# Kernel tuning notes

Measured on AMD Instinct MI355X. Metric: run time of the kernel, lower is better.

Reference implementation:

```python
import jax, jax.numpy as jnp
import numpy as np

B, S, D_MODEL, H, D_HEAD = 4, 2048, 1024, 16, 64
SCALE = D_HEAD ** -0.5


def setup_inputs() -> dict:
    key = jax.random.key(0)
    ks = jax.random.split(key, 6)
    init = lambda k, shp: jax.random.normal(k, shp, jnp.float32) * (shp[0] ** -0.5)
    Xq = jax.random.normal(ks[0], (B, S, D_MODEL), jnp.float32)
    # pre-softmax bool mask: True = masked (fill -inf) -> causal
    mask_bef = jnp.triu(jnp.ones((S, S), dtype=bool), k=1)
    # post-softmax bool mask: True = zero out that attention weight
    mask_aft = jax.random.bernoulli(ks[1], 0.1, (S, S))
    Wq = init(ks[2], (D_MODEL, H * D_HEAD))
    Wk = init(ks[3], (D_MODEL, H * D_HEAD))
    Wv = init(ks[4], (D_MODEL, H * D_HEAD))
    Wo = init(ks[5], (H * D_HEAD, D_MODEL))
    return {"Xq": Xq, "mask_bef": mask_bef, "mask_aft": mask_aft,
            "Wq": Wq, "Wk": Wk, "Wv": Wv, "Wo": Wo}


def reference(Xq, mask_bef, mask_aft, Wq, Wk, Wv, Wo):
    # Self-attention: Xk = Xv = Xq
    def split_heads(X, W):  # [B,S,D] @ [D,H*d] -> [B,H,S,d]
        return (X @ W).reshape(B, S, H, D_HEAD).transpose(0, 2, 1, 3)

    Q = split_heads(Xq, Wq)
    K = split_heads(Xq, Wk)
    V = split_heads(Xq, Wv)
    # scores: [B,H,Sq,Sk]
    scores = jnp.einsum('bhqd,bhkd->bhqk', Q, K) * SCALE
    scores = jnp.where(mask_bef, -jnp.inf, scores)  # pre-softmax bool mask
    attn = jax.nn.softmax(scores, axis=-1)
    attn = jnp.where(mask_aft, 0.0, attn)           # post-softmax bool mask
    out = jnp.einsum('bhqk,bhkd->bhqd', attn, V)    # [B,H,S,d]
    out = out.transpose(0, 2, 1, 3).reshape(B, S, H * D_HEAD)
    return out @ Wo  # [B,S,out_dim_o]
```

## Files before the change

### kernel.cpp

```cpp
#include <hip/hip_runtime.h>
#include <hip/hip_bf16.h>


using bf16 = __hip_bfloat16;
typedef __attribute__((ext_vector_type(8))) short short8;
typedef __attribute__((ext_vector_type(4))) float floatx4;

#define kB 4
#define kS 2048
#define kDM 1024
#define kH 16
#define kDH 64
#define kHeadElems ((size_t)kB * kH * kS * kDH)
#define STR 72

#if __has_builtin(__builtin_amdgcn_exp2f)
#define EXP2(x) __builtin_amdgcn_exp2f(x)
#else
#define EXP2(x) __expf((x) * 0.69314718056f)
#endif

__device__ __forceinline__ unsigned short f2bf(float f) {
    union { float f; unsigned u; } x{f};
    unsigned r = x.u + 0x7fff + ((x.u >> 16) & 1);
    return (unsigned short)(r >> 16);
}
__device__ __forceinline__ void gl_lds16(const void* g, void* l) {
    __builtin_amdgcn_global_load_lds(
        (const __attribute__((address_space(1))) unsigned int*)g,
        (__attribute__((address_space(3))) unsigned int*)l, 16, 0, 0);
}

__global__ __launch_bounds__(256)
void pack_em(const int* __restrict__ mask_aft, unsigned short* __restrict__ EM)
{
    const size_t i = ((size_t)blockIdx.x * 256 + threadIdx.x) * 8;
    const int q  = (int)(i >> 11);
    const int k0 = (int)(i & 2047);
    const int4 m0 = *(const int4*)(mask_aft + i);
    const int4 m1 = *(const int4*)(mask_aft + i + 4);
    union { unsigned short u[8]; uint4 v; } o;
    o.u[0] = (m0.x || (k0 + 0) > q) ? 0 : 0xFFFFu;
    o.u[1] = (m0.y || (k0 + 1) > q) ? 0 : 0xFFFFu;
    o.u[2] = (m0.z || (k0 + 2) > q) ? 0 : 0xFFFFu;
    o.u[3] = (m0.w || (k0 + 3) > q) ? 0 : 0xFFFFu;
    o.u[4] = (m1.x || (k0 + 4) > q) ? 0 : 0xFFFFu;
    o.u[5] = (m1.y || (k0 + 5) > q) ? 0 : 0xFFFFu;
    o.u[6] = (m1.z || (k0 + 6) > q) ? 0 : 0xFFFFu;
    o.u[7] = (m1.w || (k0 + 7) > q) ? 0 : 0xFFFFu;
    *(uint4*)(EM + i) = o.v;
}

__global__ __launch_bounds__(256)
void conv_x(const float* __restrict__ X, bf16* __restrict__ Xb)
{
    const size_t i = ((size_t)blockIdx.x * 256 + threadIdx.x) * 8;
    const float4 a = *(const float4*)(X + i);
    const float4 b = *(const float4*)(X + i + 4);
    union { unsigned short u[8]; uint4 v; } o;
    o.u[0] = f2bf(a.x); o.u[1] = f2bf(a.y); o.u[2] = f2bf(a.z); o.u[3] = f2bf(a.w);
    o.u[4] = f2bf(b.x); o.u[5] = f2bf(b.y); o.u[6] = f2bf(b.z); o.u[7] = f2bf(b.w);
    *(uint4*)(Xb + i) = o.v;
}

__global__ __launch_bounds__(256)
void conv_wT(const float* __restrict__ W, bf16* __restrict__ WT)
{
    __shared__ unsigned short Ls[64][STR];
    const int k0 = blockIdx.x * 64, n0 = blockIdx.y * 64;
    const int tid = threadIdx.x;
    const int r16 = tid >> 4, c4 = (tid & 15) * 4;
    #pragma unroll
    for (int it = 0; it < 4; ++it) {
        const int r = it * 16 + r16;
        const float4 v = *(const float4*)(W + (size_t)(k0 + r) * kDM + n0 + c4);
        Ls[c4 + 0][r] = f2bf(v.x); Ls[c4 + 1][r] = f2bf(v.y);
        Ls[c4 + 2][r] = f2bf(v.z); Ls[c4 + 3][r] = f2bf(v.w);
    }
    __syncthreads();
    #pragma unroll
    for (int it = 0; it < 4; ++it) {
        const int rn = it * 16 + r16;
        ushort4 u;
        u.x = Ls[rn][c4 + 0]; u.y = Ls[rn][c4 + 1];
        u.z = Ls[rn][c4 + 2]; u.w = Ls[rn][c4 + 3];
        *(ushort4*)(WT + (size_t)(n0 + rn) * kDM + k0 + c4) = u;
    }
}

__global__ __launch_bounds__(256)
void qkv_mfma(const bf16* __restrict__ A, const bf16* __restrict__ BT,
              bf16* __restrict__ ws)
{
    __shared__ __align__(16) unsigned short At[128][32];
    __shared__ __align__(16) unsigned short Bt[128][32];
    const int tid = threadIdx.x;
    const int w = tid >> 6, lane = tid & 63;
    const int quad = (tid >> 4) & 3, col = tid & 15;
    const int wm = w >> 1, wn = w & 1;
    const int n0 = blockIdx.x * 128;
    const int m0 = blockIdx.y * 128;

    const bf16* pA = A  + (size_t)(m0 + w * 32 + (lane >> 2)) * kDM + (lane & 3) * 8;
    const bf16* pB = BT + (size_t)(n0 + w * 32 + (lane >> 2)) * kDM + (lane & 3) * 8;
    unsigned short* lA = &At[w * 32][0];
    unsigned short* lB = &Bt[w * 32][0];

    floatx4 acc[4][4];
    #pragma unroll
    for (int i = 0; i < 4; ++i)
        #pragma unroll
        for (int j = 0; j < 4; ++j) acc[i][j] = (floatx4){0.f, 0.f, 0.f, 0.f};

    for (int k0 = 0; k0 < kDM; k0 += 32) {
        __syncthreads();
        gl_lds16(pA + k0, lA);
        gl_lds16(pA + k0 + 16 * kDM, lA + 16 * 32);
        gl_lds16(pB + k0, lB);
        gl_lds16(pB + k0 + 16 * kDM, lB + 16 * 32);
        __syncthreads();
        short8 aA[4], bB[4];
        #pragma unroll
        for (int i = 0; i < 4; ++i)
            aA[i] = *(const short8*)&At[wm * 64 + i * 16 + col][quad * 8];
        #pragma unroll
        for (int j = 0; j < 4; ++j)
            bB[j] = *(const short8*)&Bt[wn * 64 + j * 16 + col][quad * 8];
        #pragma unroll
        for (int i = 0; i < 4; ++i)
            #pragma unroll
            for (int j = 0; j < 4; ++j)
                acc[i][j] = __builtin_amdgcn_mfma_f32_16x16x32_bf16(aA[i], bB[j], acc[i][j], 0, 0, 0);
    }

    const int p  = n0 >> 10;
    const int nn = n0 & 1023;
    const float scl = (p == 0) ? 0.18033688f : 1.0f;
    bf16* Out = ws + (size_t)p * kHeadElems;
    #pragma unroll
    for (int i = 0; i < 4; ++i) {
        #pragma unroll
        for (int r = 0; r < 4; ++r) {
            const int m = m0 + wm * 64 + i * 16 + quad * 4 + r;
            const int b = m >> 11, s = m & 2047;
            #pragma unroll
            for (int j = 0; j < 4; ++j) {
                const int n = nn + wn * 64 + j * 16 + col;
                const int h = n >> 6, d = n & 63;
                Out[((size_t)(b * kH + h) * kS + s) * kDH + d] = __float2bfloat16(acc[i][j][r] * scl);
            }
        }
    }
}

__global__ __launch_bounds__(256)
void vtrans(const bf16* __restrict__ V, bf16* __restrict__ VT)
{
    const int bh = blockIdx.y;
    const int s0 = blockIdx.x * 64;
    const bf16* src = V + (size_t)bh * kS * kDH;
    bf16* dst = VT + (size_t)bh * kS * kDH;
    __shared__ unsigned short L[64][STR];
    const int tid = threadIdx.x;
    #pragma unroll
    for (int t = 0; t < 2; ++t) {
        const int idx = t * 256 + tid;
        const int r = idx >> 3, c8 = (idx & 7) * 8;
        *(uint4*)&L[r][c8] = *(const uint4*)(src + (size_t)(s0 + r) * kDH + c8);
    }
    __syncthreads();
    #pragma unroll
    for (int t = 0; t < 2; ++t) {
        const int idx = t * 256 + tid;
        const int d = idx >> 3, sc = (idx & 7) * 8;
        unsigned short tmp[8];
        #pragma unroll
        for (int e = 0; e < 8; ++e) tmp[e] = L[sc + e][d];
        *(uint4*)(dst + (size_t)d * kS + s0 + sc) = *(uint4*)tmp;
    }
}

__global__ __launch_bounds__(256, 3)
void attn_mfma(const bf16* __restrict__ ws, const bf16* __restrict__ VT,
               const unsigned short* __restrict__ EM,
               bf16* __restrict__ Aout)
{
    const int flat = blockIdx.x + blockIdx.y * 16;
    const int xcd = flat & 7;
    const int idx = flat >> 3;
    const int bh  = xcd * 8 + (idx & 7);
    const int j   = idx >> 3;
    const int qtile = (j & 1) ? (j >> 1) : (15 - (j >> 1));
    const int q0 = qtile * 128;

    const int b = bh >> 4, h = bh & 15;
    const int tid  = threadIdx.x;
    const int w    = tid >> 6;
    const int lane = tid & 63;
    const int quad = (tid >> 4) & 3;
    const int col  = tid & 15;

    const size_t ho = (size_t)bh * kS * kDH;
    const bf16* Qg  = ws + ho;
    const bf16* Kg  = ws + kHeadElems + ho;
    const bf16* VTg = VT + ho;

    __shared__ __align__(16) unsigned short Ks[2][64][64];
    __shared__ __align__(16) unsigned short Vs[2][64][64];
    __shared__ __align__(16) unsigned short Pw[4][2][16][STR];

    const int qw = q0 + w * 32;
    const int swz = col & 7;
    const int sch = (lane & 7) ^ (lane >> 3);

    short8 bQ[2][2];
    const unsigned short* EMq[2];
    #pragma unroll
    for (int sub = 0; sub < 2; ++sub) {
        const bf16* qrow = Qg + (size_t)(qw + sub * 16 + col) * kDH;
        bQ[sub][0] = *(const short8*)(qrow + quad * 8);
        bQ[sub][1] = *(const short8*)(qrow + 32 + quad * 8);
        EMq[sub] = EM + (size_t)(qw + sub * 16 + col) * kS;
    }

    floatx4 Ov[2][4];
    #pragma unroll
    for (int sub = 0; sub < 2; ++sub)
        #pragma unroll
        for (int dg = 0; dg < 4; ++dg) Ov[sub][dg] = (floatx4){0.f, 0.f, 0.f, 0.f};
    float lacc[2] = {0.f, 0.f};

    const int nt = qtile * 2 + 2;

    auto STAGE = [&](int buf, int kt) {
        const bf16* Kt = Kg  + (size_t)(kt * 64) * kDH;
        const bf16* Vt = VTg + kt * 64;
        #pragma unroll
        for (int t = 0; t < 2; ++t) {
            const int rbase = (t * 4 + w) * 8;
            const int r = rbase + (lane >> 3);
            gl_lds16(Kt + (size_t)r * kDH + sch * 8, &Ks[buf][rbase][0]);
            gl_lds16(Vt + (size_t)r * kS  + sch * 8, &Vs[buf][rbase][0]);
        }
    };

    STAGE(0, 0);
    asm volatile("s_waitcnt vmcnt(0)" ::: "memory");
    __builtin_amdgcn_s_barrier();
    __builtin_amdgcn_sched_barrier(0);

    int cur = 0;
    for (int kt = 0; kt < nt; ++kt) {
        if (kt + 1 < nt) STAGE(cur ^ 1, kt + 1);

        const int kt64 = kt * 64;
        if (kt64 <= qw + 31) {
            floatx4 sg[2][4];
            __builtin_amdgcn_s_setprio(1);
            #pragma unroll
            for (int g = 0; g < 4; ++g) {
                const int krow = g * 16 + col;
                const short8 aK0 = *(const short8*)&Ks[cur][krow][(quad ^ swz) * 8];
                const short8 aK1 = *(const short8*)&Ks[cur][krow][((4 + quad) ^ swz) * 8];
                floatx4 sA = {0.f, 0.f, 0.f, 0.f}, sB = {0.f, 0.f, 0.f, 0.f};
                sA = __builtin_amdgcn_mfma_f32_16x16x32_bf16(aK0, bQ[0][0], sA, 0, 0, 0);
                sA = __builtin_amdgcn_mfma_f32_16x16x32_bf16(aK1, bQ[0][1], sA, 0, 0, 0);
                sB = __builtin_amdgcn_mfma_f32_16x16x32_bf16(aK0, bQ[1][0], sB, 0, 0, 0);
                sB = __builtin_amdgcn_mfma_f32_16x16x32_bf16(aK1, bQ[1][1], sB, 0, 0, 0);
                sg[0][g] = sA; sg[1][g] = sB;
            }
            __builtin_amdgcn_s_setprio(0);

            #pragma unroll
            for (int sub = 0; sub < 2; ++sub) {
                const int qbase = qw + sub * 16;
                const bool needC = (kt64 + 63 > qbase);
                float lc = 0.f;
                #pragma unroll
                for (int g = 0; g < 4; ++g) {
                    const float p0 = EXP2(sg[sub][g][0]);
                    const float p1 = EXP2(sg[sub][g][1]);
                    const float p2 = EXP2(sg[sub][g][2]);
                    const float p3 = EXP2(sg[sub][g][3]);
                    if (needC) {
                        const int kb = kt64 + g * 16 + quad * 4;
                        const int qme = qbase + col;
                        lc += (kb + 0 <= qme) ? p0 : 0.f;
                        lc += (kb + 1 <= qme) ? p1 : 0.f;
                        lc += (kb + 2 <= qme) ? p2 : 0.f;
                        lc += (kb + 3 <= qme) ? p3 : 0.f;
                    } else {
                        lc += (p0 + p1) + (p2 + p3);
                    }
                    const unsigned b0 = __float_as_uint(p0) + 0x8000u;
                    const unsigned b1 = __float_as_uint(p1) + 0x8000u;
                    const unsigned b2 = __float_as_uint(p2) + 0x8000u;
                    const unsigned b3 = __float_as_uint(p3) + 0x8000u;
                    uint2 pk;
                    pk.x = __builtin_amdgcn_perm(b1, b0, 0x07060302u);
                    pk.y = __builtin_amdgcn_perm(b3, b2, 0x07060302u);
                    const uint2 em = *(const uint2*)(EMq[sub] + kt64 + g * 16 + quad * 4);
                    pk.x &= em.x; pk.y &= em.y;
                    *(uint2*)&Pw[w][sub][col][g * 16 + quad * 4] = pk;
                }
                lacc[sub] += lc;
            }

            const short8 aP[2][2] = {
                { *(const short8*)&Pw[w][0][col][quad * 8],
                  *(const short8*)&Pw[w][0][col][32 + quad * 8] },
                { *(const short8*)&Pw[w][1][col][quad * 8],
                  *(const short8*)&Pw[w][1][col][32 + quad * 8] } };
            __builtin_amdgcn_s_setprio(1);
            #pragma unroll
            for (int dg = 0; dg < 4; ++dg) {
                const int vrow = dg * 16 + col;
                const short8 bV0 = *(const short8*)&Vs[cur][vrow][(quad ^ swz) * 8];
                const short8 bV1 = *(const short8*)&Vs[cur][vrow][((4 + quad) ^ swz) * 8];
                Ov[0][dg] = __builtin_amdgcn_mfma_f32_16x16x32_bf16(aP[0][0], bV0, Ov[0][dg], 0, 0, 0);
                Ov[0][dg] = __builtin_amdgcn_mfma_f32_16x16x32_bf16(aP[0][1], bV1, Ov[0][dg], 0, 0, 0);
                Ov[1][dg] = __builtin_amdgcn_mfma_f32_16x16x32_bf16(aP[1][0], bV0, Ov[1][dg], 0, 0, 0);
                Ov[1][dg] = __builtin_amdgcn_mfma_f32_16x16x32_bf16(aP[1][1], bV1, Ov[1][dg], 0, 0, 0);
            }
            __builtin_amdgcn_s_setprio(0);
        }

        asm volatile("s_waitcnt vmcnt(0)" ::: "memory");
        __builtin_amdgcn_s_barrier();
        __builtin_amdgcn_sched_barrier(0);
        cur ^= 1;
    }

    #pragma unroll
    for (int sub = 0; sub < 2; ++sub) {
        float l = lacc[sub];
        l += __shfl_xor(l, 16, 64);
        l += __shfl_xor(l, 32, 64);
        const float linv = 1.f / l;
        #pragma unroll
        for (int r = 0; r < 4; ++r) {
            const float sc = __shfl(linv, quad * 4 + r, 64);
            const int q = qw + sub * 16 + quad * 4 + r;
            bf16* orow = Aout + ((size_t)(b * kS + q)) * kDM + h * kDH;
            #pragma unroll
            for (int dg = 0; dg < 4; ++dg)
                orow[dg * 16 + col] = __float2bfloat16(Ov[sub][dg][r] * sc);
        }
    }
}

__global__ __launch_bounds__(256)
void out_mfma(const bf16* __restrict__ A, const bf16* __restrict__ BT,
              float* __restrict__ Out)
{
    __shared__ __align__(16) unsigned short At[128][32];
    __shared__ __align__(16) unsigned short Bt[128][32];
    const int tid = threadIdx.x;
    const int w = tid >> 6, lane = tid & 63;
    const int quad = (tid >> 4) & 3, col = tid & 15;
    const int wm = w >> 1, wn = w & 1;
    const int n0 = blockIdx.x * 128;
    const int m0 = blockIdx.y * 128;

    const bf16* pA = A  + (size_t)(m0 + w * 32 + (lane >> 2)) * kDM + (lane & 3) * 8;
    const bf16* pB = BT + (size_t)(n0 + w * 32 + (lane >> 2)) * kDM + (lane & 3) * 8;
    unsigned short* lA = &At[w * 32][0];
    unsigned short* lB = &Bt[w * 32][0];

    floatx4 acc[4][4];
    #pragma unroll
    for (int i = 0; i < 4; ++i)
        #pragma unroll
        for (int j = 0; j < 4; ++j) acc[i][j] = (floatx4){0.f, 0.f, 0.f, 0.f};

    for (int k0 = 0; k0 < kDM; k0 += 32) {
        __syncthreads();
        gl_lds16(pA + k0, lA);
        gl_lds16(pA + k0 + 16 * kDM, lA + 16 * 32);
        gl_lds16(pB + k0, lB);
        gl_lds16(pB + k0 + 16 * kDM, lB + 16 * 32);
        __syncthreads();
        short8 aA[4], bB[4];
        #pragma unroll
        for (int i = 0; i < 4; ++i)
            aA[i] = *(const short8*)&At[wm * 64 + i * 16 + col][quad * 8];
        #pragma unroll
        for (int j = 0; j < 4; ++j)
            bB[j] = *(const short8*)&Bt[wn * 64 + j * 16 + col][quad * 8];
        #pragma unroll
        for (int i = 0; i < 4; ++i)
            #pragma unroll
            for (int j = 0; j < 4; ++j)
                acc[i][j] = __builtin_amdgcn_mfma_f32_16x16x32_bf16(aA[i], bB[j], acc[i][j], 0, 0, 0);
    }

    #pragma unroll
    for (int i = 0; i < 4; ++i)
        #pragma unroll
        for (int r = 0; r < 4; ++r) {
            const int m = m0 + wm * 64 + i * 16 + quad * 4 + r;
            #pragma unroll
            for (int j = 0; j < 4; ++j)
                Out[(size_t)m * kDM + n0 + wn * 64 + j * 16 + col] = acc[i][j][r];
        }
}

extern "C" void kernel_launch(void* const* d_in, const int* in_sizes, int n_in,
                              void* d_out, int out_size, void* d_ws, size_t ws_size,
                              hipStream_t stream)
{
    const float* Xq       = (const float*)d_in[0];
    const int*   mask_aft = (const int*)d_in[2];
    const float* Wq       = (const float*)d_in[3];
    const float* Wk       = (const float*)d_in[4];
    const float* Wv       = (const float*)d_in[5];
    const float* Wo       = (const float*)d_in[6];
    float* out = (float*)d_out;

    bf16* ws   = (bf16*)d_ws;
    bf16* Xbf  = ws + 3 * kHeadElems;
    bf16* Aout = Xbf;
    bf16* WoT  = ws;

    bf16* WcatT = (bf16*)d_out + 262144;
    bf16* VT    = (bf16*)((char*)d_out + 8u * 1024 * 1024);
    unsigned short* EMp = (unsigned short*)((char*)d_out + 24u * 1024 * 1024);

    pack_em <<<dim3(2048), 256, 0, stream>>>(mask_aft, EMp);
    conv_x  <<<dim3(4096), 256, 0, stream>>>(Xq, Xbf);
    conv_wT <<<dim3(16, 16), 256, 0, stream>>>(Wq, WcatT);
    conv_wT <<<dim3(16, 16), 256, 0, stream>>>(Wk, WcatT + (size_t)kDM * kDM);
    conv_wT <<<dim3(16, 16), 256, 0, stream>>>(Wv, WcatT + 2 * (size_t)kDM * kDM);
    qkv_mfma<<<dim3(24, 64), 256, 0, stream>>>(Xbf, WcatT, ws);
    vtrans  <<<dim3(32, 64), 256, 0, stream>>>(ws + 2 * kHeadElems, VT);
    attn_mfma<<<dim3(16, 64), 256, 0, stream>>>(ws, VT, EMp, Aout);
    conv_wT <<<dim3(16, 16), 256, 0, stream>>>(Wo, WoT);
    out_mfma<<<dim3(8, 64), 256, 0, stream>>>(Aout, WoT, out);
}
```

Before: 340.2 us.

## Remap blocks for XCD locality, hoist mask loads, use packed bf16 convert

The QKV GEMM now assigns its 24 column tiles three per XCD, so each XCD's L2 shares B-tiles. The attention kernel's q-tile ordering is changed to a different causal load-balancing pattern. The attention loop prefetches the post-softmax mask words before staging the next K/V tile, and replaces manual round-and-perm bf16 packing with v_cvt_pk_bf16_f32. The out GEMM's block index mapping is rewritten but is effectively the same row-major order. The packed convert rounds to nearest-even rather than the old add-0x8000 rounding, and the hoisted mask values use extra registers.

```diff
diff --git a/kernel.cpp b/kernel.cpp
--- a/kernel.cpp
+++ b/kernel.cpp
@@ -24,6 +24,11 @@
     union { float f; unsigned u; } x{f};
     unsigned r = x.u + 0x7fff + ((x.u >> 16) & 1);
     return (unsigned short)(r >> 16);
+}
+__device__ __forceinline__ unsigned cvt_pk_bf16(float lo, float hi) {
+    unsigned r;
+    asm("v_cvt_pk_bf16_f32 %0, %1, %2" : "=v"(r) : "v"(lo), "v"(hi));
+    return r;
 }
 __device__ __forceinline__ void gl_lds16(const void* g, void* l) {
     __builtin_amdgcn_global_load_lds(
@@ -98,8 +103,11 @@
     const int w = tid >> 6, lane = tid & 63;
     const int quad = (tid >> 4) & 3, col = tid & 15;
     const int wm = w >> 1, wn = w & 1;
-    const int n0 = blockIdx.x * 128;
-    const int m0 = blockIdx.y * 128;
+    const int flat = blockIdx.x + blockIdx.y * 24;
+    const int xcd = flat & 7;
+    const int i2 = flat >> 3;
+    const int n0 = (xcd * 3 + (i2 % 3)) * 128;
+    const int m0 = (i2 / 3) * 128;
 
     const bf16* pA = A  + (size_t)(m0 + w * 32 + (lane >> 2)) * kDM + (lane & 3) * 8;
     const bf16* pB = BT + (size_t)(n0 + w * 32 + (lane >> 2)) * kDM + (lane & 3) * 8;
@@ -190,7 +198,8 @@
     const int idx = flat >> 3;
     const int bh  = xcd * 8 + (idx & 7);
     const int j   = idx >> 3;
-    const int qtile = (j & 1) ? (j >> 1) : (15 - (j >> 1));
+    const int kk  = 3 - (j >> 2);
+    const int qtile = 4 * kk + ((kk + (j & 3)) & 3);
     const int q0 = qtile * 128;
 
     const int b = bh >> 4, h = bh & 15;
@@ -251,10 +260,22 @@
 
     int cur = 0;
     for (int kt = 0; kt < nt; ++kt) {
+        const int kt64 = kt * 64;
+        const bool doC = (kt64 <= qw + 31);
+
+        uint2 em[2][4];
+        if (doC) {
+            #pragma unroll
+            for (int sub = 0; sub < 2; ++sub)
+                #pragma unroll
+                for (int g = 0; g < 4; ++g)
+                    em[sub][g] = *(const uint2*)(EMq[sub] + kt64 + g * 16 + quad * 4);
+            __builtin_amdgcn_sched_barrier(0);
+        }
+
         if (kt + 1 < nt) STAGE(cur ^ 1, kt + 1);
 
-        const int kt64 = kt * 64;
-        if (kt64 <= qw + 31) {
+        if (doC) {
             floatx4 sg[2][4];
             __builtin_amdgcn_s_setprio(1);
             #pragma unroll
@@ -292,15 +313,9 @@
                     } else {
                         lc += (p0 + p1) + (p2 + p3);
                     }
-                    const unsigned b0 = __float_as_uint(p0) + 0x8000u;
-                    const unsigned b1 = __float_as_uint(p1) + 0x8000u;
-                    const unsigned b2 = __float_as_uint(p2) + 0x8000u;
-                    const unsigned b3 = __float_as_uint(p3) + 0x8000u;
                     uint2 pk;
-                    pk.x = __builtin_amdgcn_perm(b1, b0, 0x07060302u);
-                    pk.y = __builtin_amdgcn_perm(b3, b2, 0x07060302u);
-                    const uint2 em = *(const uint2*)(EMq[sub] + kt64 + g * 16 + quad * 4);
-                    pk.x &= em.x; pk.y &= em.y;
+                    pk.x = cvt_pk_bf16(p0, p1) & em[sub][g].x;
+                    pk.y = cvt_pk_bf16(p2, p3) & em[sub][g].y;
                     *(uint2*)&Pw[w][sub][col][g * 16 + quad * 4] = pk;
                 }
                 lacc[sub] += lc;
@@ -359,8 +374,9 @@
     const int w = tid >> 6, lane = tid & 63;
     const int quad = (tid >> 4) & 3, col = tid & 15;
     const int wm = w >> 1, wn = w & 1;
-    const int n0 = blockIdx.x * 128;
-    const int m0 = blockIdx.y * 128;
+    const int flat = blockIdx.x + blockIdx.y * 8;
+    const int n0 = (flat & 7) * 128;
+    const int m0 = (flat >> 3) * 128;
 
     const bf16* pA = A  + (size_t)(m0 + w * 32 + (lane >> 2)) * kDM + (lane & 3) * 8;
     const bf16* pB = BT + (size_t)(n0 + w * 32 + (lane >> 2)) * kDM + (lane & 3) * 8;
```

New measurement: 323.9 us. 1.05x faster.
